# Kernel tuning notes

Measured on AMD Instinct MI355X. Metric: run time of the kernel, lower is better.

## Reference

```python
import jax, jax.numpy as jnp
import numpy as np

H = 4       # N_head
C = 32      # c_hidden
CZ = 128    # c_z
N = 256
B = 1
EPS = 1e-5


def setup_inputs() -> dict:
    key = jax.random.key(0)
    ks = jax.random.split(key, 8)
    hc = H * C
    return {
        "z": jax.random.normal(ks[0], (B, N, N, CZ), dtype=jnp.float32),
        "ln_scale": jnp.ones((CZ,), dtype=jnp.float32),
        "ln_bias": jnp.zeros((CZ,), dtype=jnp.float32),
        "Wq": jax.random.normal(ks[1], (CZ, hc), dtype=jnp.float32) * 0.02,
        "Wk": jax.random.normal(ks[2], (CZ, hc), dtype=jnp.float32) * 0.02,
        "Wv": jax.random.normal(ks[3], (CZ, hc), dtype=jnp.float32) * 0.02,
        "Wb": jax.random.normal(ks[4], (CZ, H), dtype=jnp.float32) * 0.02,
        "Wg": jax.random.normal(ks[5], (CZ, hc), dtype=jnp.float32) * 0.02,
        "Wo": jax.random.normal(ks[6], (hc, CZ), dtype=jnp.float32) * 0.02,
    }


def reference(z, ln_scale, ln_bias, Wq, Wk, Wv, Wb, Wg, Wo):
    b, n = z.shape[0], z.shape[1]
    # LayerNorm over c_z
    mu = jnp.mean(z, axis=-1, keepdims=True)
    var = jnp.mean(jnp.square(z - mu), axis=-1, keepdims=True)
    zn = (z - mu) * jax.lax.rsqrt(var + EPS) * ln_scale + ln_bias
    # projections -> [B, N, N, H, C]
    q = (zn @ Wq).reshape(b, n, n, H, C)
    k = (zn @ Wk).reshape(b, n, n, H, C)
    v = (zn @ Wv).reshape(b, n, n, H, C)
    bias = zn @ Wb                                  # [B, N, N, H]
    g = jax.nn.sigmoid(zn @ Wg).reshape(b, n, n, H, C)
    # attention around starting node i: query at (i,j), keys/values at (i,k)
    scores = jnp.einsum('bijhd,bikhd->bijkh', q, k) * (1.0 / C ** 0.5)
    scores = scores + bias[:, None, :, :, :]        # bias[b, j, k, h]
    a = jax.nn.softmax(scores, axis=-2)             # softmax over k
    o = jnp.einsum('bijkh,bikhd->bijhd', a, v)      # [B, N, N, H, C]
    o = (g * o).reshape(b, n, n, H * C)
    return o @ Wo
```

## Files before the change

### kernel.cpp

```cpp
#include <hip/hip_runtime.h>
#include <math.h>

#define NN 256
#define CZ 128
#define NH 4
#define CH 32
#define HC 128
#define NPIX (NN*NN)
#define L2E   1.4426950408889634f
#define SCALE2 (0.17677669529663687f * 1.4426950408889634f)

typedef __attribute__((ext_vector_type(8))) short bf16x8;
typedef __attribute__((ext_vector_type(4))) float fx4;
typedef __attribute__((ext_vector_type(4))) unsigned u32x4;

__device__ __forceinline__ unsigned pack_hl(float x) {
    unsigned b  = __builtin_bit_cast(unsigned, x);
    unsigned hb = b & 0xFFFF0000u;
    float r = x - __builtin_bit_cast(float, hb);
    return hb | (__builtin_bit_cast(unsigned, r) >> 16);
}
__device__ __forceinline__ void load_split8(const float* p, bf16x8& h, bf16x8& l) {
    float4 x0 = *(const float4*)p;
    float4 x1 = *(const float4*)(p + 4);
    float xs[8] = {x0.x, x0.y, x0.z, x0.w, x1.x, x1.y, x1.z, x1.w};
    #pragma unroll
    for (int j = 0; j < 8; ++j) {
        unsigned b  = __builtin_bit_cast(unsigned, xs[j]);
        unsigned hb = b & 0xFFFF0000u;
        float r = xs[j] - __builtin_bit_cast(float, hb);
        h[j] = (short)(hb >> 16);
        l[j] = (short)(__builtin_bit_cast(unsigned, r) >> 16);
    }
}
__device__ __forceinline__ void deint8(const unsigned* p, bf16x8& h, bf16x8& l) {
    u32x4 e0 = *(const u32x4*)p;
    u32x4 e1 = *(const u32x4*)(p + 4);
    unsigned es[8] = {e0[0], e0[1], e0[2], e0[3], e1[0], e1[1], e1[2], e1[3]};
    unsigned hw[4], lw[4];
    #pragma unroll
    for (int j = 0; j < 4; ++j) {
        unsigned a = es[2 * j], b = es[2 * j + 1];
        hw[j] = (a >> 16) | (b & 0xFFFF0000u);
        lw[j] = (a & 0x0000FFFFu) | (b << 16);
    }
    h = __builtin_bit_cast(bf16x8, u32x4{hw[0], hw[1], hw[2], hw[3]});
    l = __builtin_bit_cast(bf16x8, u32x4{lw[0], lw[1], lw[2], lw[3]});
}

__global__ __launch_bounds__(256) void pack_w_kernel(
    const float* __restrict__ Wq, const float* __restrict__ Wk,
    const float* __restrict__ Wv, const float* __restrict__ Wg,
    const float* __restrict__ Wo, bf16x8* __restrict__ pk)
{
    int id  = blockIdx.x * 256 + threadIdx.x;
    int mid = id >> 11;
    int e   = id & 2047;
    const float* W = (mid == 0) ? Wq : (mid == 1) ? Wk : (mid == 2) ? Wv : (mid == 3) ? Wg : Wo;
    int quad = e & 3, n = (e >> 2) & 127, ks = e >> 9;
    int k0 = ks * 32 + quad * 8;
    bf16x8 h, l;
    #pragma unroll
    for (int j = 0; j < 8; ++j) {
        float x = W[(size_t)(k0 + j) * 128 + n];
        unsigned b  = __builtin_bit_cast(unsigned, x);
        unsigned hb = b & 0xFFFF0000u;
        float r = x - __builtin_bit_cast(float, hb);
        h[j] = (short)(hb >> 16);
        l[j] = (short)(__builtin_bit_cast(unsigned, r) >> 16);
    }
    pk[(size_t)mid * 4096 + e]        = h;
    pk[(size_t)mid * 4096 + 2048 + e] = l;
}

__global__ __launch_bounds__(256) void ln_proj_kernel(
    const float* __restrict__ z, const float* __restrict__ ls, const float* __restrict__ lb,
    const float* __restrict__ Wb, const bf16x8* __restrict__ pk,
    unsigned* __restrict__ q_pk, unsigned* __restrict__ k_pk, unsigned* __restrict__ v_pk,
    float* __restrict__ g_ws, float* __restrict__ bias_n)
{
    __shared__ float zsh[32][132];
    __shared__ float rsum[256], rsq[256];
    __shared__ float pmu[32], prs[32];

    const int t  = threadIdx.x;
    const int p0 = blockIdx.x * 32;
    const int i  = p0 >> 8;
    const int j0 = p0 & 255;

    const float4* z4 = (const float4*)(z + (size_t)p0 * CZ);
    #pragma unroll
    for (int r = 0; r < 4; ++r) {
        int idx4 = t + 256 * r;
        int p = idx4 >> 5, pos = idx4 & 31;
        *(float4*)&zsh[p][pos * 4] = z4[idx4];
    }
    __syncthreads();

    {
        int p = t >> 3, sg = t & 7;
        float s = 0.f, q = 0.f;
        #pragma unroll
        for (int u = 0; u < 16; ++u) { float x = zsh[p][sg * 16 + u]; s += x; q += x * x; }
        rsum[t] = s; rsq[t] = q;
    }
    __syncthreads();
    if (t < 32) {
        float s = 0.f, q = 0.f;
        #pragma unroll
        for (int g = 0; g < 8; ++g) { s += rsum[t * 8 + g]; q += rsq[t * 8 + g]; }
        float mu  = s * (1.0f / 128.0f);
        float var = q * (1.0f / 128.0f) - mu * mu;
        float a   = var + 1e-5f;
        float r   = rsqrtf(a);
        r = r * (1.5f - 0.5f * a * r * r);
        pmu[t] = mu; prs[t] = r;
    }
    __syncthreads();

    #pragma unroll
    for (int r4 = 0; r4 < 4; ++r4) {
        int idx4 = t + 256 * r4;
        int p = idx4 >> 5, pos = idx4 & 31;
        float4 v  = *(float4*)&zsh[p][pos * 4];
        float4 s4 = ((const float4*)ls)[pos];
        float4 b4 = ((const float4*)lb)[pos];
        float mu = pmu[p], rs = prs[p];
        v.x = (v.x - mu) * rs * s4.x + b4.x;
        v.y = (v.y - mu) * rs * s4.y + b4.y;
        v.z = (v.z - mu) * rs * s4.z + b4.z;
        v.w = (v.w - mu) * rs * s4.w + b4.w;
        *(float4*)&zsh[p][pos * 4] = v;
    }
    __syncthreads();

    const int wv = t >> 6, lane = t & 63;
    const int lrow = lane & 15, quad = lane >> 4;
    const bf16x8* ph = pk + (size_t)wv * 4096;
    const bf16x8* pl = ph + 2048;

    fx4 acc[2][8];
    #pragma unroll
    for (int mr = 0; mr < 2; ++mr)
        #pragma unroll
        for (int nc = 0; nc < 8; ++nc)
            acc[mr][nc] = fx4{0.f, 0.f, 0.f, 0.f};

    #pragma unroll
    for (int ks = 0; ks < 4; ++ks) {
        bf16x8 ah[2], al[2];
        #pragma unroll
        for (int mr = 0; mr < 2; ++mr)
            load_split8(&zsh[mr * 16 + lrow][ks * 32 + quad * 8], ah[mr], al[mr]);
        #pragma unroll
        for (int nc = 0; nc < 8; ++nc) {
            int bi = (ks * 128 + nc * 16 + lrow) * 4 + quad;
            bf16x8 bh = ph[bi], bl = pl[bi];
            #pragma unroll
            for (int mr = 0; mr < 2; ++mr) {
                acc[mr][nc] = __builtin_amdgcn_mfma_f32_16x16x32_bf16(ah[mr], bl, acc[mr][nc], 0, 0, 0);
                acc[mr][nc] = __builtin_amdgcn_mfma_f32_16x16x32_bf16(al[mr], bh, acc[mr][nc], 0, 0, 0);
                acc[mr][nc] = __builtin_amdgcn_mfma_f32_16x16x32_bf16(ah[mr], bh, acc[mr][nc], 0, 0, 0);
            }
        }
    }

    #pragma unroll
    for (int mr = 0; mr < 2; ++mr) {
        #pragma unroll
        for (int nc = 0; nc < 8; ++nc) {
            int cg = nc * 16 + lrow;
            int h = cg >> 5, cc = cg & 31;
            int jl = mr * 16 + quad * 4;
            fx4 a = acc[mr][nc];
            if (wv == 0) {
                unsigned* qp = q_pk + ((size_t)(i * NH + h) * NN + j0 + jl) * CH + cc;
                #pragma unroll
                for (int r = 0; r < 4; ++r) qp[r * CH] = pack_hl(a[r]);
            } else if (wv == 1) {
                unsigned* kp = k_pk + ((size_t)(i * NH + h) * NN + j0 + jl) * CH + cc;
                #pragma unroll
                for (int r = 0; r < 4; ++r) kp[r * CH] = pack_hl(a[r]);
            } else if (wv == 2) {
                u32x4 e = {pack_hl(a[0]), pack_hl(a[1]), pack_hl(a[2]), pack_hl(a[3])};
                *(u32x4*)(v_pk + ((size_t)(i * NH + h) * CH + cc) * NN + j0 + jl) = e;
            } else {
                float* gp = g_ws + (size_t)(p0 + jl) * HC + cg;
                #pragma unroll
                for (int r = 0; r < 4; ++r) gp[r * HC] = 1.0f / (1.0f + __expf(-a[r]));
            }
        }
    }

    if (t < 128) {
        int hh = t >> 5, p = t & 31;
        float b = 0.f;
        for (int d = 0; d < 128; ++d) b = fmaf(zsh[p][d], Wb[d * 4 + hh], b);
        bias_n[(size_t)hh * NPIX + (size_t)i * NN + j0 + p] = b * L2E;
    }
}

#define PSTR 40
__global__ __launch_bounds__(256) void attn_kernel(
    const unsigned* __restrict__ q_pk, const unsigned* __restrict__ k_pk,
    const unsigned* __restrict__ v_pk, const float* __restrict__ g_ws,
    const float* __restrict__ bias_n, float* __restrict__ go_ws)
{
    __shared__ unsigned short Psh[4][2][64 * PSTR];

    const int t = threadIdx.x;
    const int wv = t >> 6, lane = t & 63;
    const int lrow = lane & 15, quad = lane >> 4;
    const int h = blockIdx.x & 3, i = blockIdx.x >> 2;
    const int qb = wv * 64;

    const unsigned* qs = q_pk + (size_t)(i * NH + h) * NN * CH;
    const unsigned* ks = k_pk + (size_t)(i * NH + h) * NN * CH;
    const unsigned* vs = v_pk + (size_t)(i * NH + h) * CH * NN;
    const float*    bs = bias_n + (size_t)h * NPIX;

    bf16x8 qh[4], ql[4];
    #pragma unroll
    for (int nt = 0; nt < 4; ++nt)
        deint8(qs + (size_t)(qb + nt * 16 + lrow) * CH + quad * 8, qh[nt], ql[nt]);

    fx4 oacc[2][4];
    #pragma unroll
    for (int ct = 0; ct < 2; ++ct)
        #pragma unroll
        for (int nt = 0; nt < 4; ++nt)
            oacc[ct][nt] = fx4{0.f, 0.f, 0.f, 0.f};
    float lsum[4] = {0.f, 0.f, 0.f, 0.f};

    for (int kb = 0; kb < NN; kb += 32) {
        bf16x8 kh[2], kl_[2];
        #pragma unroll
        for (int mt = 0; mt < 2; ++mt)
            deint8(ks + (size_t)(kb + mt * 16 + lrow) * CH + quad * 8, kh[mt], kl_[mt]);
        bf16x8 vh[2], vl[2];
        #pragma unroll
        for (int ct = 0; ct < 2; ++ct)
            deint8(vs + (size_t)(ct * 16 + lrow) * NN + kb + quad * 8, vh[ct], vl[ct]);

        #pragma unroll
        for (int nt = 0; nt < 4; ++nt) {
            #pragma unroll
            for (int mt = 0; mt < 2; ++mt) {
                float4 bv = *(const float4*)(bs + (size_t)(qb + nt * 16 + lrow) * NN
                                                + kb + mt * 16 + quad * 4);

                fx4 sv = fx4{0.f, 0.f, 0.f, 0.f};
                sv = __builtin_amdgcn_mfma_f32_16x16x32_bf16(kh[mt], ql[nt], sv, 0, 0, 0);
                sv = __builtin_amdgcn_mfma_f32_16x16x32_bf16(kl_[mt], qh[nt], sv, 0, 0, 0);
                sv = __builtin_amdgcn_mfma_f32_16x16x32_bf16(kh[mt], qh[nt], sv, 0, 0, 0);

                float e0 = exp2f(fmaf(sv[0], SCALE2, bv.x));
                float e1 = exp2f(fmaf(sv[1], SCALE2, bv.y));
                float e2 = exp2f(fmaf(sv[2], SCALE2, bv.z));
                float e3 = exp2f(fmaf(sv[3], SCALE2, bv.w));
                lsum[nt] += (e0 + e1) + (e2 + e3);

                unsigned b0 = __builtin_bit_cast(unsigned, e0);
                unsigned b1 = __builtin_bit_cast(unsigned, e1);
                unsigned b2 = __builtin_bit_cast(unsigned, e2);
                unsigned b3 = __builtin_bit_cast(unsigned, e3);
                unsigned h01 = (b0 >> 16) | (b1 & 0xFFFF0000u);
                unsigned h23 = (b2 >> 16) | (b3 & 0xFFFF0000u);
                float r0 = e0 - __builtin_bit_cast(float, b0 & 0xFFFF0000u);
                float r1 = e1 - __builtin_bit_cast(float, b1 & 0xFFFF0000u);
                float r2 = e2 - __builtin_bit_cast(float, b2 & 0xFFFF0000u);
                float r3 = e3 - __builtin_bit_cast(float, b3 & 0xFFFF0000u);
                unsigned l01 = (__builtin_bit_cast(unsigned, r0) >> 16)
                             | (__builtin_bit_cast(unsigned, r1) & 0xFFFF0000u);
                unsigned l23 = (__builtin_bit_cast(unsigned, r2) >> 16)
                             | (__builtin_bit_cast(unsigned, r3) & 0xFFFF0000u);

                int wo = (nt * 16 + lrow) * PSTR + mt * 16 + quad * 4;
                *(uint2*)&Psh[wv][0][wo] = make_uint2(h01, h23);
                *(uint2*)&Psh[wv][1][wo] = make_uint2(l01, l23);
            }
        }

        #pragma unroll
        for (int nt = 0; nt < 4; ++nt) {
            bf16x8 pbh = *(const bf16x8*)&Psh[wv][0][(nt * 16 + lrow) * PSTR + quad * 8];
            bf16x8 pbl = *(const bf16x8*)&Psh[wv][1][(nt * 16 + lrow) * PSTR + quad * 8];
            #pragma unroll
            for (int ct = 0; ct < 2; ++ct) {
                oacc[ct][nt] = __builtin_amdgcn_mfma_f32_16x16x32_bf16(vh[ct], pbl, oacc[ct][nt], 0, 0, 0);
                oacc[ct][nt] = __builtin_amdgcn_mfma_f32_16x16x32_bf16(vl[ct], pbh, oacc[ct][nt], 0, 0, 0);
                oacc[ct][nt] = __builtin_amdgcn_mfma_f32_16x16x32_bf16(vh[ct], pbh, oacc[ct][nt], 0, 0, 0);
            }
        }
    }

    #pragma unroll
    for (int nt = 0; nt < 4; ++nt) {
        float s = lsum[nt];
        s += __shfl_xor(s, 16, 64);
        s += __shfl_xor(s, 32, 64);
        float inv = 1.0f / s;
        size_t pix = (size_t)i * NN + qb + nt * 16 + lrow;
        #pragma unroll
        for (int ct = 0; ct < 2; ++ct) {
            const float* gp = g_ws + pix * HC + h * CH + ct * 16 + quad * 4;
            float4 g4 = *(const float4*)gp;
            fx4 o = oacc[ct][nt];
            float4 r;
            r.x = g4.x * o[0] * inv;
            r.y = g4.y * o[1] * inv;
            r.z = g4.z * o[2] * inv;
            r.w = g4.w * o[3] * inv;
            *(float4*)(go_ws + pix * HC + h * CH + ct * 16 + quad * 4) = r;
        }
    }
}

__global__ __launch_bounds__(256) void outproj_kernel(
    const float* __restrict__ go_ws, const bf16x8* __restrict__ pk, float* __restrict__ out)
{
    __shared__ float gsh[64][132];
    const int t  = threadIdx.x;
    const int p0 = blockIdx.x * 64;

    const float4* g4 = (const float4*)(go_ws + (size_t)p0 * HC);
    #pragma unroll
    for (int r = 0; r < 8; ++r) {
        int idx4 = t + 256 * r;
        int p = idx4 >> 5, pos = idx4 & 31;
        *(float4*)&gsh[p][pos * 4] = g4[idx4];
    }
    __syncthreads();

    const int wv = t >> 6, lane = t & 63;
    const int lrow = lane & 15, quad = lane >> 4;
    const bf16x8* ph = pk + (size_t)4 * 4096;
    const bf16x8* pl = ph + 2048;

    fx4 acc[8];
    #pragma unroll
    for (int nc = 0; nc < 8; ++nc) acc[nc] = fx4{0.f, 0.f, 0.f, 0.f};

    #pragma unroll
    for (int ks = 0; ks < 4; ++ks) {
        bf16x8 ah, al;
        load_split8(&gsh[wv * 16 + lrow][ks * 32 + quad * 8], ah, al);
        #pragma unroll
        for (int nc = 0; nc < 8; ++nc) {
            int bi = (ks * 128 + nc * 16 + lrow) * 4 + quad;
            bf16x8 bh = ph[bi], bl = pl[bi];
            acc[nc] = __builtin_amdgcn_mfma_f32_16x16x32_bf16(ah, bl, acc[nc], 0, 0, 0);
            acc[nc] = __builtin_amdgcn_mfma_f32_16x16x32_bf16(al, bh, acc[nc], 0, 0, 0);
            acc[nc] = __builtin_amdgcn_mfma_f32_16x16x32_bf16(ah, bh, acc[nc], 0, 0, 0);
        }
    }

    #pragma unroll
    for (int nc = 0; nc < 8; ++nc) {
        #pragma unroll
        for (int r = 0; r < 4; ++r)
            out[(size_t)(p0 + wv * 16 + quad * 4 + r) * HC + nc * 16 + lrow] = acc[nc][r];
    }
}

extern "C" void kernel_launch(void* const* d_in, const int* in_sizes, int n_in,
                              void* d_out, int out_size, void* d_ws, size_t ws_size,
                              hipStream_t stream)
{
    const float* z  = (const float*)d_in[0];
    const float* ls = (const float*)d_in[1];
    const float* lb = (const float*)d_in[2];
    const float* Wq = (const float*)d_in[3];
    const float* Wk = (const float*)d_in[4];
    const float* Wv = (const float*)d_in[5];
    const float* Wb = (const float*)d_in[6];
    const float* Wg = (const float*)d_in[7];
    const float* Wo = (const float*)d_in[8];

    float* ws = (float*)d_ws;
    const size_t BIG = (size_t)NPIX * HC;
    unsigned* q_pk  = (unsigned*)ws;
    unsigned* k_pk  = (unsigned*)(ws + BIG);
    unsigned* v_pk  = (unsigned*)(ws + 2 * BIG);
    float* g_ws     = ws + 3 * BIG;
    float* go_ws    = ws + 4 * BIG;
    float* bias_n   = ws + 5 * BIG;
    bf16x8* pk      = (bf16x8*)(bias_n + (size_t)NH * NPIX);

    pack_w_kernel<<<40, 256, 0, stream>>>(Wq, Wk, Wv, Wg, Wo, pk);
    ln_proj_kernel<<<NPIX / 32, 256, 0, stream>>>(z, ls, lb, Wb, pk,
                                                  q_pk, k_pk, v_pk, g_ws, bias_n);
    attn_kernel<<<NN * NH, 256, 0, stream>>>(q_pk, k_pk, v_pk, g_ws, bias_n, go_ws);
    outproj_kernel<<<NPIX / 64, 256, 0, stream>>>(go_ws, pk, (float*)d_out);
}
```

Baseline: 247.3 us.

## Store q/k/v as split hi/lo planes and pre-tile bias into MFMA fragment order

The projection kernel now writes the bf16 high and low halves of q, k and v into separate planar arrays instead of interleaved 32-bit words. The attention kernel can then load MFMA operands directly without per-element deinterleave shuffles. The pair bias is stored in an order that matches the MFMA fragment, so each lane reads a contiguous float4 with a simple stride. The change also uses v_perm for packing P and adds an occupancy hint to launch_bounds. The narrower 16-bit scattered stores in the projection kernel may cost more store transactions.

```diff
diff --git a/kernel.cpp b/kernel.cpp
--- a/kernel.cpp
+++ b/kernel.cpp
@@ -12,13 +12,13 @@
 
 typedef __attribute__((ext_vector_type(8))) short bf16x8;
 typedef __attribute__((ext_vector_type(4))) float fx4;
-typedef __attribute__((ext_vector_type(4))) unsigned u32x4;
-
-__device__ __forceinline__ unsigned pack_hl(float x) {
+
+__device__ __forceinline__ void split1(float x, short& h, short& l) {
     unsigned b  = __builtin_bit_cast(unsigned, x);
     unsigned hb = b & 0xFFFF0000u;
     float r = x - __builtin_bit_cast(float, hb);
-    return hb | (__builtin_bit_cast(unsigned, r) >> 16);
+    h = (short)(hb >> 16);
+    l = (short)(__builtin_bit_cast(unsigned, r) >> 16);
 }
 __device__ __forceinline__ void load_split8(const float* p, bf16x8& h, bf16x8& l) {
     float4 x0 = *(const float4*)p;
@@ -26,26 +26,10 @@
     float xs[8] = {x0.x, x0.y, x0.z, x0.w, x1.x, x1.y, x1.z, x1.w};
     #pragma unroll
     for (int j = 0; j < 8; ++j) {
-        unsigned b  = __builtin_bit_cast(unsigned, xs[j]);
-        unsigned hb = b & 0xFFFF0000u;
-        float r = xs[j] - __builtin_bit_cast(float, hb);
-        h[j] = (short)(hb >> 16);
-        l[j] = (short)(__builtin_bit_cast(unsigned, r) >> 16);
-    }
-}
-__device__ __forceinline__ void deint8(const unsigned* p, bf16x8& h, bf16x8& l) {
-    u32x4 e0 = *(const u32x4*)p;
-    u32x4 e1 = *(const u32x4*)(p + 4);
-    unsigned es[8] = {e0[0], e0[1], e0[2], e0[3], e1[0], e1[1], e1[2], e1[3]};
-    unsigned hw[4], lw[4];
-    #pragma unroll
-    for (int j = 0; j < 4; ++j) {
-        unsigned a = es[2 * j], b = es[2 * j + 1];
-        hw[j] = (a >> 16) | (b & 0xFFFF0000u);
-        lw[j] = (a & 0x0000FFFFu) | (b << 16);
-    }
-    h = __builtin_bit_cast(bf16x8, u32x4{hw[0], hw[1], hw[2], hw[3]});
-    l = __builtin_bit_cast(bf16x8, u32x4{lw[0], lw[1], lw[2], lw[3]});
+        short hh, ll;
+        split1(xs[j], hh, ll);
+        h[j] = hh; l[j] = ll;
+    }
 }
 
 __global__ __launch_bounds__(256) void pack_w_kernel(
@@ -63,11 +47,9 @@
     #pragma unroll
     for (int j = 0; j < 8; ++j) {
         float x = W[(size_t)(k0 + j) * 128 + n];
-        unsigned b  = __builtin_bit_cast(unsigned, x);
-        unsigned hb = b & 0xFFFF0000u;
-        float r = x - __builtin_bit_cast(float, hb);
-        h[j] = (short)(hb >> 16);
-        l[j] = (short)(__builtin_bit_cast(unsigned, r) >> 16);
+        short hh, ll;
+        split1(x, hh, ll);
+        h[j] = hh; l[j] = ll;
     }
     pk[(size_t)mid * 4096 + e]        = h;
     pk[(size_t)mid * 4096 + 2048 + e] = l;
@@ -76,8 +58,10 @@
 __global__ __launch_bounds__(256) void ln_proj_kernel(
     const float* __restrict__ z, const float* __restrict__ ls, const float* __restrict__ lb,
     const float* __restrict__ Wb, const bf16x8* __restrict__ pk,
-    unsigned* __restrict__ q_pk, unsigned* __restrict__ k_pk, unsigned* __restrict__ v_pk,
-    float* __restrict__ g_ws, float* __restrict__ bias_n)
+    short* __restrict__ q_h, short* __restrict__ q_l,
+    short* __restrict__ k_h, short* __restrict__ k_l,
+    short* __restrict__ v_h, short* __restrict__ v_l,
+    float* __restrict__ g_ws, float* __restrict__ bias_f)
 {
     __shared__ float zsh[32][132];
     __shared__ float rsum[256], rsq[256];
@@ -173,17 +157,24 @@
             int h = cg >> 5, cc = cg & 31;
             int jl = mr * 16 + quad * 4;
             fx4 a = acc[mr][nc];
-            if (wv == 0) {
-                unsigned* qp = q_pk + ((size_t)(i * NH + h) * NN + j0 + jl) * CH + cc;
+            if (wv == 0 || wv == 1) {
+                size_t base = ((size_t)(i * NH + h) * NN + j0 + jl) * CH + cc;
+                short* dh = (wv == 0 ? q_h : k_h) + base;
+                short* dl = (wv == 0 ? q_l : k_l) + base;
                 #pragma unroll
-                for (int r = 0; r < 4; ++r) qp[r * CH] = pack_hl(a[r]);
-            } else if (wv == 1) {
-                unsigned* kp = k_pk + ((size_t)(i * NH + h) * NN + j0 + jl) * CH + cc;
-                #pragma unroll
-                for (int r = 0; r < 4; ++r) kp[r * CH] = pack_hl(a[r]);
+                for (int r = 0; r < 4; ++r) {
+                    short hs, lo; split1(a[r], hs, lo);
+                    dh[r * CH] = hs; dl[r * CH] = lo;
+                }
             } else if (wv == 2) {
-                u32x4 e = {pack_hl(a[0]), pack_hl(a[1]), pack_hl(a[2]), pack_hl(a[3])};
-                *(u32x4*)(v_pk + ((size_t)(i * NH + h) * CH + cc) * NN + j0 + jl) = e;
+                size_t base = ((size_t)(i * NH + h) * CH + cc) * NN + j0 + jl;
+                short4 hv, lv;
+                split1(a[0], hv.x, lv.x);
+                split1(a[1], hv.y, lv.y);
+                split1(a[2], hv.z, lv.z);
+                split1(a[3], hv.w, lv.w);
+                *(short4*)(v_h + base) = hv;
+                *(short4*)(v_l + base) = lv;
             } else {
                 float* gp = g_ws + (size_t)(p0 + jl) * HC + cg;
                 #pragma unroll
@@ -196,15 +187,19 @@
         int hh = t >> 5, p = t & 31;
         float b = 0.f;
         for (int d = 0; d < 128; ++d) b = fmaf(zsh[p][d], Wb[d * 4 + hh], b);
-        bias_n[(size_t)hh * NPIX + (size_t)i * NN + j0 + p] = b * L2E;
+        int jt = i >> 4, lrowb = i & 15;
+        int kt = (j0 + p) >> 4, quadb = (p >> 2) & 3, rr = p & 3;
+        bias_f[(((size_t)(hh * 16 + jt) * 16 + kt) * 64 + quadb * 16 + lrowb) * 4 + rr] = b * L2E;
     }
 }
 
 #define PSTR 40
-__global__ __launch_bounds__(256) void attn_kernel(
-    const unsigned* __restrict__ q_pk, const unsigned* __restrict__ k_pk,
-    const unsigned* __restrict__ v_pk, const float* __restrict__ g_ws,
-    const float* __restrict__ bias_n, float* __restrict__ go_ws)
+__global__ __launch_bounds__(256, 4) void attn_kernel(
+    const short* __restrict__ q_h, const short* __restrict__ q_l,
+    const short* __restrict__ k_h, const short* __restrict__ k_l,
+    const short* __restrict__ v_h, const short* __restrict__ v_l,
+    const float* __restrict__ g_ws, const float* __restrict__ bias_f,
+    float* __restrict__ go_ws)
 {
     __shared__ unsigned short Psh[4][2][64 * PSTR];
 
@@ -214,15 +209,19 @@
     const int h = blockIdx.x & 3, i = blockIdx.x >> 2;
     const int qb = wv * 64;
 
-    const unsigned* qs = q_pk + (size_t)(i * NH + h) * NN * CH;
-    const unsigned* ks = k_pk + (size_t)(i * NH + h) * NN * CH;
-    const unsigned* vs = v_pk + (size_t)(i * NH + h) * CH * NN;
-    const float*    bs = bias_n + (size_t)h * NPIX;
+    const size_t slab  = (size_t)(i * NH + h) * NN * CH;
+    const short* qsh = q_h + slab;  const short* qsl = q_l + slab;
+    const short* ksh = k_h + slab;  const short* ksl = k_l + slab;
+    const short* vsh = v_h + slab;  const short* vsl = v_l + slab;
+    const float* bbase = bias_f + (size_t)(h * 16 + wv * 4) * 4096 + lane * 4;
 
     bf16x8 qh[4], ql[4];
     #pragma unroll
-    for (int nt = 0; nt < 4; ++nt)
-        deint8(qs + (size_t)(qb + nt * 16 + lrow) * CH + quad * 8, qh[nt], ql[nt]);
+    for (int nt = 0; nt < 4; ++nt) {
+        size_t o = (size_t)(qb + nt * 16 + lrow) * CH + quad * 8;
+        qh[nt] = *(const bf16x8*)(qsh + o);
+        ql[nt] = *(const bf16x8*)(qsl + o);
+    }
 
     fx4 oacc[2][4];
     #pragma unroll
@@ -233,21 +232,27 @@
     float lsum[4] = {0.f, 0.f, 0.f, 0.f};
 
     for (int kb = 0; kb < NN; kb += 32) {
+        const int kt0 = kb >> 4;
         bf16x8 kh[2], kl_[2];
         #pragma unroll
-        for (int mt = 0; mt < 2; ++mt)
-            deint8(ks + (size_t)(kb + mt * 16 + lrow) * CH + quad * 8, kh[mt], kl_[mt]);
+        for (int mt = 0; mt < 2; ++mt) {
+            size_t o = (size_t)(kb + mt * 16 + lrow) * CH + quad * 8;
+            kh[mt]  = *(const bf16x8*)(ksh + o);
+            kl_[mt] = *(const bf16x8*)(ksl + o);
+        }
         bf16x8 vh[2], vl[2];
         #pragma unroll
-        for (int ct = 0; ct < 2; ++ct)
-            deint8(vs + (size_t)(ct * 16 + lrow) * NN + kb + quad * 8, vh[ct], vl[ct]);
+        for (int ct = 0; ct < 2; ++ct) {
+            size_t o = (size_t)(ct * 16 + lrow) * NN + kb + quad * 8;
+            vh[ct] = *(const bf16x8*)(vsh + o);
+            vl[ct] = *(const bf16x8*)(vsl + o);
+        }
 
         #pragma unroll
         for (int nt = 0; nt < 4; ++nt) {
             #pragma unroll
             for (int mt = 0; mt < 2; ++mt) {
-                float4 bv = *(const float4*)(bs + (size_t)(qb + nt * 16 + lrow) * NN
-                                                + kb + mt * 16 + quad * 4);
+                float4 bv = *(const float4*)(bbase + (size_t)(nt * 16 + kt0 + mt) * 256);
 
                 fx4 sv = fx4{0.f, 0.f, 0.f, 0.f};
                 sv = __builtin_amdgcn_mfma_f32_16x16x32_bf16(kh[mt], ql[nt], sv, 0, 0, 0);
@@ -264,16 +269,16 @@
                 unsigned b1 = __builtin_bit_cast(unsigned, e1);
                 unsigned b2 = __builtin_bit_cast(unsigned, e2);
                 unsigned b3 = __builtin_bit_cast(unsigned, e3);
-                unsigned h01 = (b0 >> 16) | (b1 & 0xFFFF0000u);
-                unsigned h23 = (b2 >> 16) | (b3 & 0xFFFF0000u);
+                unsigned h01 = __builtin_amdgcn_perm(b1, b0, 0x07060302u);
+                unsigned h23 = __builtin_amdgcn_perm(b3, b2, 0x07060302u);
                 float r0 = e0 - __builtin_bit_cast(float, b0 & 0xFFFF0000u);
                 float r1 = e1 - __builtin_bit_cast(float, b1 & 0xFFFF0000u);
                 float r2 = e2 - __builtin_bit_cast(float, b2 & 0xFFFF0000u);
                 float r3 = e3 - __builtin_bit_cast(float, b3 & 0xFFFF0000u);
-                unsigned l01 = (__builtin_bit_cast(unsigned, r0) >> 16)
-                             | (__builtin_bit_cast(unsigned, r1) & 0xFFFF0000u);
-                unsigned l23 = (__builtin_bit_cast(unsigned, r2) >> 16)
-                             | (__builtin_bit_cast(unsigned, r3) & 0xFFFF0000u);
+                unsigned l01 = __builtin_amdgcn_perm(__builtin_bit_cast(unsigned, r1),
+                                                     __builtin_bit_cast(unsigned, r0), 0x07060302u);
+                unsigned l23 = __builtin_amdgcn_perm(__builtin_bit_cast(unsigned, r3),
+                                                     __builtin_bit_cast(unsigned, r2), 0x07060302u);
 
                 int wo = (nt * 16 + lrow) * PSTR + mt * 16 + quad * 4;
                 *(uint2*)&Psh[wv][0][wo] = make_uint2(h01, h23);
@@ -379,17 +384,22 @@
 
     float* ws = (float*)d_ws;
     const size_t BIG = (size_t)NPIX * HC;
-    unsigned* q_pk  = (unsigned*)ws;
-    unsigned* k_pk  = (unsigned*)(ws + BIG);
-    unsigned* v_pk  = (unsigned*)(ws + 2 * BIG);
-    float* g_ws     = ws + 3 * BIG;
-    float* go_ws    = ws + 4 * BIG;
-    float* bias_n   = ws + 5 * BIG;
-    bf16x8* pk      = (bf16x8*)(bias_n + (size_t)NH * NPIX);
+    short* q_h = (short*)ws;
+    short* q_l = q_h + BIG;
+    short* k_h = q_l + BIG;
+    short* k_l = k_h + BIG;
+    short* v_h = k_l + BIG;
+    short* v_l = v_h + BIG;
+    float* g_ws   = ws + 3 * BIG;
+    float* go_ws  = ws + 4 * BIG;
+    float* bias_f = ws + 5 * BIG;
+    bf16x8* pk    = (bf16x8*)(bias_f + (size_t)NH * NPIX);
 
     pack_w_kernel<<<40, 256, 0, stream>>>(Wq, Wk, Wv, Wg, Wo, pk);
     ln_proj_kernel<<<NPIX / 32, 256, 0, stream>>>(z, ls, lb, Wb, pk,
-                                                  q_pk, k_pk, v_pk, g_ws, bias_n);
-    attn_kernel<<<NN * NH, 256, 0, stream>>>(q_pk, k_pk, v_pk, g_ws, bias_n, go_ws);
+                                                  q_h, q_l, k_h, k_l, v_h, v_l,
+                                                  g_ws, bias_f);
+    attn_kernel<<<NN * NH, 256, 0, stream>>>(q_h, q_l, k_h, k_l, v_h, v_l,
+                                             g_ws, bias_f, go_ws);
     outproj_kernel<<<NPIX / 64, 256, 0, stream>>>(go_ws, pk, (float*)d_out);
 }
```

New measurement: 252.5 us. 2.1% more time.
